# Kernel optimization log

Hardware: AMD Instinct MI355X
Metric: run time of the kernel (lower is better)

The kernel has to match this reference:

```python
import jax, jax.numpy as jnp
import numpy as np

HEADS = 12
EMBED = 768
HEAD_DIM = EMBED // HEADS


def setup_inputs() -> dict:
    key = jax.random.key(0)
    kx, kw, kb = jax.random.split(key, 3)
    x = jax.random.normal(kx, (8, 1024, EMBED), dtype=jnp.float32)
    # nn.Linear(embed, 3*embed): weight (3E, E), bias (3E,)
    W_qkv = jax.random.normal(kw, (3 * EMBED, EMBED), dtype=jnp.float32) * (1.0 / np.sqrt(EMBED))
    b_qkv = jax.random.normal(kb, (3 * EMBED,), dtype=jnp.float32) * 0.01
    return {"x": x, "W_qkv": W_qkv, "b_qkv": b_qkv}


def reference(x, W_qkv, b_qkv):
    b, n, e = x.shape
    qkv = x @ W_qkv.T + b_qkv                       # (b, n, 3E)
    qkv = qkv.reshape(b, n, HEADS, 3 * HEAD_DIM)    # (b, n, h, 3d)
    q, k, v = jnp.split(qkv, 3, axis=-1)            # each (b, n, h, d)
    scores = jnp.einsum('bihd,bjhd->bijh', q, k) / np.sqrt(HEAD_DIM)
    attn = jax.nn.softmax(scores, axis=-2)          # softmax over keys j (dim=-2)
    out = jnp.einsum('bijh,bjhd->bihd', attn, v)
    return out.reshape(b, n, e)
```

## Files before the change

### kernel.cpp

```cpp
#include <hip/hip_runtime.h>
#include <hip/hip_bf16.h>
#include <cstdint>

#define BATCH 8
#define SEQ   1024
#define EMB   768
#define HEADS 12
#define HDIM  64
#define C3    2304
#define MROWS (BATCH*SEQ)
#define KSLC  (EMB / 16)
#define XPACK_BLOCKS (MROWS * KSLC / 256)
#define WPACK_BLOCKS (C3 * KSLC / 256)

typedef __attribute__((ext_vector_type(8)))  short bf16x8;
typedef __attribute__((ext_vector_type(4)))  short bf16x4;
typedef __attribute__((ext_vector_type(4)))  float f32x4;
typedef __attribute__((ext_vector_type(16))) float f32x16;

static __device__ inline short f2bf(float f) {
    union { float f; uint32_t u; } v; v.f = f;
    uint32_t u = v.u + 0x7fff + ((v.u >> 16) & 1);
    return (short)(u >> 16);
}

__global__ __launch_bounds__(256) void pack_bf16(const float* __restrict__ x,
                                                 short* __restrict__ xb2,
                                                 const float* __restrict__ W,
                                                 short* __restrict__ Wb2) {
    const float* in;
    short* out;
    int tid;
    if (blockIdx.x < XPACK_BLOCKS) {
        in = x; out = xb2;
        tid = blockIdx.x * 256 + threadIdx.x;
    } else {
        in = W; out = Wb2;
        tid = (blockIdx.x - XPACK_BLOCKS) * 256 + threadIdx.x;
    }
    const int r    = tid & 31;
    const int ks   = (tid >> 5) % KSLC;
    const int tile = tid / (KSLC * 32);
    const int row  = tile * 32 + r;

    const float* src = in + (size_t)row * EMB + ks * 16;
    float4 v0 = ((const float4*)src)[0];
    float4 v1 = ((const float4*)src)[1];
    float4 v2 = ((const float4*)src)[2];
    float4 v3 = ((const float4*)src)[3];
    bf16x8 o0 = { f2bf(v0.x), f2bf(v0.y), f2bf(v0.z), f2bf(v0.w),
                  f2bf(v1.x), f2bf(v1.y), f2bf(v1.z), f2bf(v1.w) };
    bf16x8 o1 = { f2bf(v2.x), f2bf(v2.y), f2bf(v2.z), f2bf(v2.w),
                  f2bf(v3.x), f2bf(v3.y), f2bf(v3.z), f2bf(v3.w) };
    short* dst = out + (size_t)tid * 16;
    *(bf16x8*)(dst)     = o0;
    *(bf16x8*)(dst + 8) = o1;
}

__global__ __launch_bounds__(256) void qkv_gemm_mfma(const short* __restrict__ xb2,
                                                     const short* __restrict__ Wb2,
                                                     const float* __restrict__ bias,
                                                     short* __restrict__ qkvb) {
    const int g    = blockIdx.x;
    const int xcd  = g & 7;
    const int ring = g >> 3;
    const int by   = xcd * 8 + (ring & 7);
    const int bx   = ring >> 3;

    const int t = threadIdx.x;
    const int w = t >> 6;
    const int lane = t & 63;
    const int l5  = lane >> 5;
    const int r31 = lane & 31;
    const int m0 = by * 128, n0 = bx * 128;
    const int wm = (w & 1) * 64, wn = (w >> 1) * 64;

    const int laneoff = r31 * 16 + l5 * 8;
    const short* pa0 = xb2 + ((size_t)((m0 + wm) >> 5) * KSLC) * 512 + laneoff;
    const short* pa1 = pa0 + (size_t)KSLC * 512;
    const short* pb0 = Wb2 + ((size_t)((n0 + wn) >> 5) * KSLC) * 512 + laneoff;
    const short* pb1 = pb0 + (size_t)KSLC * 512;

    f32x16 acc[2][2] = {};

    #pragma unroll 4
    for (int ks = 0; ks < KSLC; ++ks) {
        bf16x8 a0 = *(const bf16x8*)(pa0 + ks * 512);
        bf16x8 a1 = *(const bf16x8*)(pa1 + ks * 512);
        bf16x8 b0 = *(const bf16x8*)(pb0 + ks * 512);
        bf16x8 b1 = *(const bf16x8*)(pb1 + ks * 512);
        acc[0][0] = __builtin_amdgcn_mfma_f32_32x32x16_bf16(a0, b0, acc[0][0], 0, 0, 0);
        acc[0][1] = __builtin_amdgcn_mfma_f32_32x32x16_bf16(a0, b1, acc[0][1], 0, 0, 0);
        acc[1][0] = __builtin_amdgcn_mfma_f32_32x32x16_bf16(a1, b0, acc[1][0], 0, 0, 0);
        acc[1][1] = __builtin_amdgcn_mfma_f32_32x32x16_bf16(a1, b1, acc[1][1], 0, 0, 0);
    }

    float bsv[2], scl[2];
    #pragma unroll
    for (int nt = 0; nt < 2; ++nt) {
        int n = n0 + wn + nt * 32 + r31;
        bsv[nt] = bias[n];
        scl[nt] = ((n % 192) < 64) ? 0.125f : 1.0f;
    }
    #pragma unroll
    for (int mt = 0; mt < 2; ++mt)
        #pragma unroll
        for (int nt = 0; nt < 2; ++nt) {
            int n = n0 + wn + nt * 32 + r31;
            #pragma unroll
            for (int reg = 0; reg < 16; ++reg) {
                int row = (reg & 3) + 8 * (reg >> 2) + 4 * l5;
                int m = m0 + wm + mt * 32 + row;
                float v = (acc[mt][nt][reg] + bsv[nt]) * scl[nt];
                qkvb[(size_t)m * C3 + n] = f2bf(v);
            }
        }
}

__global__ __launch_bounds__(256) void v_transpose(const short* __restrict__ qkvb,
                                                   short* __restrict__ vt) {
    __shared__ int Lt[64][65];

    const int bh = blockIdx.x;
    const int jt = blockIdx.y;
    const int b = bh / HEADS, h = bh % HEADS;
    const int t = threadIdx.x;
    const int j0 = jt * 64;
    const size_t base = (size_t)b * SEQ * C3 + (size_t)h * 192 + 128;

    #pragma unroll
    for (int p = 0; p < 2; ++p) {
        int idx = p * 256 + t;
        int j = idx >> 3, d0 = (idx & 7) * 8;
        bf16x8 v = *(const bf16x8*)(qkvb + base + (size_t)(j0 + j) * C3 + d0);
        #pragma unroll
        for (int u = 0; u < 8; ++u)
            Lt[d0 + u][j] = (int)(unsigned short)v[u];
    }
    __syncthreads();
    #pragma unroll
    for (int p = 0; p < 2; ++p) {
        int idx = p * 256 + t;
        int d = idx >> 3, c8 = (idx & 7) * 8;
        bf16x8 o;
        #pragma unroll
        for (int u = 0; u < 8; ++u)
            o[u] = (short)Lt[d][c8 + u];
        *(bf16x8*)(vt + ((size_t)bh * 64 + d) * SEQ + j0 + c8) = o;
    }
}

#define LDP 72

__global__ __launch_bounds__(256, 3) void attn_mfma(const short* __restrict__ qkvb,
                                                    const short* __restrict__ vt,
                                                    float* __restrict__ out) {
    __shared__ short Ks[64][LDP];
    __shared__ short Vt[64][LDP];
    __shared__ short Ps[128][LDP];

    const int g    = blockIdx.x;
    const int qt   = g / (BATCH * HEADS);
    const int bh   = g % (BATCH * HEADS);
    const int b    = bh / HEADS;
    const int h    = bh % HEADS;
    const int t    = threadIdx.x;
    const int w    = t >> 6;
    const int lane = t & 63;
    const int c    = lane & 15;
    const int q    = lane >> 4;
    const int i0   = qt * 128;

    const size_t base = (size_t)b * SEQ * C3 + (size_t)h * 192;
    const short* vtb = vt + (size_t)bh * 64 * SEQ;

    #pragma unroll
    for (int p = 0; p < 4; ++p) {
        int idx = p * 256 + t;
        int i = idx >> 3, d0 = (idx & 7) << 3;
        *(bf16x8*)&Ps[i][d0] =
            *(const bf16x8*)(qkvb + base + (size_t)(i0 + i) * C3 + d0);
    }
    __syncthreads();
    bf16x8 aq[2][2];
    #pragma unroll
    for (int s = 0; s < 2; ++s) {
        aq[s][0] = *(bf16x8*)&Ps[w * 32 + s * 16 + c][q * 8];
        aq[s][1] = *(bf16x8*)&Ps[w * 32 + s * 16 + c][32 + q * 8];
    }

    f32x4 o[2][4] = {};
    float l_acc[2] = {0.f, 0.f};

    for (int kt = 0; kt < 16; ++kt) {
        const int j0 = kt * 64;
        __syncthreads();
        #pragma unroll
        for (int p = 0; p < 2; ++p) {
            int idx = p * 256 + t;
            int j = idx >> 3, d0 = (idx & 7) << 3;
            *(bf16x8*)&Ks[j][d0] =
                *(const bf16x8*)(qkvb + base + 64 + (size_t)(j0 + j) * C3 + d0);
        }
        #pragma unroll
        for (int p = 0; p < 2; ++p) {
            int idx = p * 256 + t;
            int d = idx >> 3, j8 = (idx & 7) << 3;
            *(bf16x8*)&Vt[d][j8] =
                *(const bf16x8*)(vtb + (size_t)d * SEQ + j0 + j8);
        }
        __syncthreads();

        bf16x8 ka[4][2];
        #pragma unroll
        for (int mt = 0; mt < 4; ++mt) {
            ka[mt][0] = *(bf16x8*)&Ks[mt * 16 + c][q * 8];
            ka[mt][1] = *(bf16x8*)&Ks[mt * 16 + c][32 + q * 8];
        }

        f32x4 s[2][4];
        #pragma unroll
        for (int ss = 0; ss < 2; ++ss)
            #pragma unroll
            for (int mt = 0; mt < 4; ++mt) {
                f32x4 acc = {0.f, 0.f, 0.f, 0.f};
                acc = __builtin_amdgcn_mfma_f32_16x16x32_bf16(ka[mt][0], aq[ss][0], acc, 0, 0, 0);
                acc = __builtin_amdgcn_mfma_f32_16x16x32_bf16(ka[mt][1], aq[ss][1], acc, 0, 0, 0);
                s[ss][mt] = acc;
            }

        #pragma unroll
        for (int ss = 0; ss < 2; ++ss)
            #pragma unroll
            for (int mt = 0; mt < 4; ++mt) {
                float p0 = __expf(s[ss][mt][0]);
                float p1 = __expf(s[ss][mt][1]);
                float p2 = __expf(s[ss][mt][2]);
                float p3 = __expf(s[ss][mt][3]);
                l_acc[ss] += (p0 + p1) + (p2 + p3);
                bf16x4 pw = { f2bf(p0), f2bf(p1), f2bf(p2), f2bf(p3) };
                *(bf16x4*)&Ps[w * 32 + ss * 16 + c][mt * 16 + 4 * q] = pw;
            }

        bf16x8 vb[4][2];
        #pragma unroll
        for (int dt = 0; dt < 4; ++dt) {
            vb[dt][0] = *(bf16x8*)&Vt[dt * 16 + c][q * 8];
            vb[dt][1] = *(bf16x8*)&Vt[dt * 16 + c][32 + q * 8];
        }

        #pragma unroll
        for (int ss = 0; ss < 2; ++ss) {
            bf16x8 ap0 = *(bf16x8*)&Ps[w * 32 + ss * 16 + c][q * 8];
            bf16x8 ap1 = *(bf16x8*)&Ps[w * 32 + ss * 16 + c][32 + q * 8];
            #pragma unroll
            for (int dt = 0; dt < 4; ++dt) {
                o[ss][dt] = __builtin_amdgcn_mfma_f32_16x16x32_bf16(ap0, vb[dt][0], o[ss][dt], 0, 0, 0);
                o[ss][dt] = __builtin_amdgcn_mfma_f32_16x16x32_bf16(ap1, vb[dt][1], o[ss][dt], 0, 0, 0);
            }
        }
    }

    float linv[2][4];
    #pragma unroll
    for (int ss = 0; ss < 2; ++ss) {
        float v = l_acc[ss];
        v += __shfl_xor(v, 16, 64);
        v += __shfl_xor(v, 32, 64);
        #pragma unroll
        for (int r = 0; r < 4; ++r)
            linv[ss][r] = 1.0f / __shfl(v, 4 * q + r, 64);
    }

    #pragma unroll
    for (int ss = 0; ss < 2; ++ss)
        #pragma unroll
        for (int dt = 0; dt < 4; ++dt)
            #pragma unroll
            for (int r = 0; r < 4; ++r) {
                int i = w * 32 + ss * 16 + q * 4 + r;
                out[((size_t)b * SEQ + i0 + i) * EMB + h * HDIM + dt * 16 + c]
                    = o[ss][dt][r] * linv[ss][r];
            }
}

extern "C" void kernel_launch(void* const* d_in, const int* in_sizes, int n_in,
                              void* d_out, int out_size, void* d_ws, size_t ws_size,
                              hipStream_t stream) {
    const float* x    = (const float*)d_in[0];
    const float* W    = (const float*)d_in[1];
    const float* bias = (const float*)d_in[2];
    float* out = (float*)d_out;

    short* xb2  = (short*)d_ws;
    short* Wb2  = xb2 + (size_t)MROWS * EMB;
    short* qkvb = Wb2 + (size_t)C3 * EMB;
    short* vt   = qkvb + (size_t)MROWS * C3;

    pack_bf16<<<XPACK_BLOCKS + WPACK_BLOCKS, 256, 0, stream>>>(x, xb2, W, Wb2);

    qkv_gemm_mfma<<<1152, 256, 0, stream>>>(xb2, Wb2, bias, qkvb);

    dim3 g2(BATCH * HEADS, SEQ / 64);
    v_transpose<<<g2, 256, 0, stream>>>(qkvb, vt);

    attn_mfma<<<BATCH * HEADS * (SEQ / 128), 256, 0, stream>>>(qkvb, vt, out);
}
```

Measured before the change: 171.1 us.

## Fuse V transpose into QKV GEMM epilogue and write head-major Q/K

The GEMM epilogue now writes Q and K into contiguous per-(batch,head) [SEQ,64] buffers and writes V directly transposed as [bh,64,SEQ] using 4-element vector stores. This removes the separate v_transpose kernel launch and its extra read and write of V. Attention Q/K tile loads become fully contiguous instead of strided by 2304. The trade-off is that Q/K stores from the epilogue are scalar shorts strided by 64 elements, which may coalesce poorly.

```diff
diff --git a/kernel.cpp b/kernel.cpp
--- a/kernel.cpp
+++ b/kernel.cpp
@@ -60,7 +60,9 @@
 __global__ __launch_bounds__(256) void qkv_gemm_mfma(const short* __restrict__ xb2,
                                                      const short* __restrict__ Wb2,
                                                      const float* __restrict__ bias,
-                                                     short* __restrict__ qkvb) {
+                                                     short* __restrict__ qb,
+                                                     short* __restrict__ kb,
+                                                     short* __restrict__ vt) {
     const int g    = blockIdx.x;
     const int xcd  = g & 7;
     const int ring = g >> 3;
@@ -95,64 +97,49 @@
         acc[1][1] = __builtin_amdgcn_mfma_f32_32x32x16_bf16(a1, b1, acc[1][1], 0, 0, 0);
     }
 
-    float bsv[2], scl[2];
+    const int b  = m0 >> 10;
+    const int mi = (m0 & 1023) + wm;
     #pragma unroll
     for (int nt = 0; nt < 2; ++nt) {
-        int n = n0 + wn + nt * 32 + r31;
-        bsv[nt] = bias[n];
-        scl[nt] = ((n % 192) < 64) ? 0.125f : 1.0f;
-    }
-    #pragma unroll
-    for (int mt = 0; mt < 2; ++mt)
-        #pragma unroll
-        for (int nt = 0; nt < 2; ++nt) {
-            int n = n0 + wn + nt * 32 + r31;
-            #pragma unroll
-            for (int reg = 0; reg < 16; ++reg) {
-                int row = (reg & 3) + 8 * (reg >> 2) + 4 * l5;
-                int m = m0 + wm + mt * 32 + row;
-                float v = (acc[mt][nt][reg] + bsv[nt]) * scl[nt];
-                qkvb[(size_t)m * C3 + n] = f2bf(v);
-            }
-        }
-}
-
-__global__ __launch_bounds__(256) void v_transpose(const short* __restrict__ qkvb,
-                                                   short* __restrict__ vt) {
-    __shared__ int Lt[64][65];
-
-    const int bh = blockIdx.x;
-    const int jt = blockIdx.y;
-    const int b = bh / HEADS, h = bh % HEADS;
-    const int t = threadIdx.x;
-    const int j0 = jt * 64;
-    const size_t base = (size_t)b * SEQ * C3 + (size_t)h * 192 + 128;
-
-    #pragma unroll
-    for (int p = 0; p < 2; ++p) {
-        int idx = p * 256 + t;
-        int j = idx >> 3, d0 = (idx & 7) * 8;
-        bf16x8 v = *(const bf16x8*)(qkvb + base + (size_t)(j0 + j) * C3 + d0);
-        #pragma unroll
-        for (int u = 0; u < 8; ++u)
-            Lt[d0 + u][j] = (int)(unsigned short)v[u];
-    }
-    __syncthreads();
-    #pragma unroll
-    for (int p = 0; p < 2; ++p) {
-        int idx = p * 256 + t;
-        int d = idx >> 3, c8 = (idx & 7) * 8;
-        bf16x8 o;
-        #pragma unroll
-        for (int u = 0; u < 8; ++u)
-            o[u] = (short)Lt[d][c8 + u];
-        *(bf16x8*)(vt + ((size_t)bh * 64 + d) * SEQ + j0 + c8) = o;
+        const int n_start = n0 + wn + nt * 32;
+        const int h    = n_start / 192;
+        const int comp = (n_start % 192) >> 6;
+        const int d    = (n_start & 63) + r31;
+        const float bv = bias[n_start + r31];
+        const float sc = (comp == 0) ? 0.125f : 1.0f;
+        const size_t bh = (size_t)(b * HEADS + h);
+
+        if (comp < 2) {
+            short* dst = (comp == 0 ? qb : kb) + bh * SEQ * 64 + d;
+            #pragma unroll
+            for (int mt = 0; mt < 2; ++mt)
+                #pragma unroll
+                for (int reg = 0; reg < 16; ++reg) {
+                    int row = (reg & 3) + 8 * (reg >> 2) + 4 * l5;
+                    int i = mi + mt * 32 + row;
+                    dst[(size_t)i * 64] = f2bf((acc[mt][nt][reg] + bv) * sc);
+                }
+        } else {
+            short* dst = vt + (bh * 64 + d) * SEQ;
+            #pragma unroll
+            for (int mt = 0; mt < 2; ++mt)
+                #pragma unroll
+                for (int gr = 0; gr < 4; ++gr) {
+                    int j0r = mi + mt * 32 + 8 * gr + 4 * l5;
+                    bf16x4 pv = { f2bf(acc[mt][nt][4 * gr + 0] + bv),
+                                  f2bf(acc[mt][nt][4 * gr + 1] + bv),
+                                  f2bf(acc[mt][nt][4 * gr + 2] + bv),
+                                  f2bf(acc[mt][nt][4 * gr + 3] + bv) };
+                    *(bf16x4*)(dst + j0r) = pv;
+                }
+        }
     }
 }
 
 #define LDP 72
 
-__global__ __launch_bounds__(256, 3) void attn_mfma(const short* __restrict__ qkvb,
+__global__ __launch_bounds__(256, 3) void attn_mfma(const short* __restrict__ qb,
+                                                    const short* __restrict__ kb,
                                                     const short* __restrict__ vt,
                                                     float* __restrict__ out) {
     __shared__ short Ks[64][LDP];
@@ -171,15 +158,15 @@
     const int q    = lane >> 4;
     const int i0   = qt * 128;
 
-    const size_t base = (size_t)b * SEQ * C3 + (size_t)h * 192;
+    const short* qbb = qb + (size_t)bh * SEQ * 64;
+    const short* kbb = kb + (size_t)bh * SEQ * 64;
     const short* vtb = vt + (size_t)bh * 64 * SEQ;
 
     #pragma unroll
     for (int p = 0; p < 4; ++p) {
         int idx = p * 256 + t;
         int i = idx >> 3, d0 = (idx & 7) << 3;
-        *(bf16x8*)&Ps[i][d0] =
-            *(const bf16x8*)(qkvb + base + (size_t)(i0 + i) * C3 + d0);
+        *(bf16x8*)&Ps[i][d0] = *(const bf16x8*)(qbb + (size_t)i0 * 64 + idx * 8);
     }
     __syncthreads();
     bf16x8 aq[2][2];
@@ -199,8 +186,7 @@
         for (int p = 0; p < 2; ++p) {
             int idx = p * 256 + t;
             int j = idx >> 3, d0 = (idx & 7) << 3;
-            *(bf16x8*)&Ks[j][d0] =
-                *(const bf16x8*)(qkvb + base + 64 + (size_t)(j0 + j) * C3 + d0);
+            *(bf16x8*)&Ks[j][d0] = *(const bf16x8*)(kbb + (size_t)j0 * 64 + idx * 8);
         }
         #pragma unroll
         for (int p = 0; p < 2; ++p) {
@@ -292,17 +278,15 @@
     const float* bias = (const float*)d_in[2];
     float* out = (float*)d_out;
 
-    short* xb2  = (short*)d_ws;
-    short* Wb2  = xb2 + (size_t)MROWS * EMB;
-    short* qkvb = Wb2 + (size_t)C3 * EMB;
-    short* vt   = qkvb + (size_t)MROWS * C3;
+    short* xb2 = (short*)d_ws;
+    short* Wb2 = xb2 + (size_t)MROWS * EMB;
+    short* qb  = Wb2 + (size_t)C3 * EMB;
+    short* kb  = qb  + (size_t)BATCH * HEADS * SEQ * HDIM;
+    short* vt  = kb  + (size_t)BATCH * HEADS * SEQ * HDIM;
 
     pack_bf16<<<XPACK_BLOCKS + WPACK_BLOCKS, 256, 0, stream>>>(x, xb2, W, Wb2);
 
-    qkv_gemm_mfma<<<1152, 256, 0, stream>>>(xb2, Wb2, bias, qkvb);
-
-    dim3 g2(BATCH * HEADS, SEQ / 64);
-    v_transpose<<<g2, 256, 0, stream>>>(qkvb, vt);
-
-    attn_mfma<<<BATCH * HEADS * (SEQ / 128), 256, 0, stream>>>(qkvb, vt, out);
-}
+    qkv_gemm_mfma<<<1152, 256, 0, stream>>>(xb2, Wb2, bias, qb, kb, vt);
+
+    attn_mfma<<<BATCH * HEADS * (SEQ / 128), 256, 0, stream>>>(qb, kb, vt, out);
+}
```

New measurement: 179.5 us. 1.05x slower.
